# Kernel tuning notes

Hardware: AMD Instinct MI355X
Metric: run time of the kernel (lower is better)

The kernel has to match this reference:

```python
import jax, jax.numpy as jnp
import numpy as np
import math

N = 1000            # proposals
C = 91              # classes incl. background (class 0)
K = 100             # num_detections per class
SCORE_TH = 0.05
NMS_TH = 0.5
MIN_SIZE = 1.0
WX, WY, WW, WH = 10.0, 10.0, 5.0, 5.0   # reg_weights
BBOX_CLIP = math.log(1000.0 / 16.0)


def setup_inputs() -> dict:
    key = jax.random.key(0)
    k1, k2, k3, k4, k5, k6 = jax.random.split(key, 6)
    class_logit = jax.random.normal(k1, (N, C), jnp.float32)
    box_regression = jax.random.normal(k2, (N, C * 4), jnp.float32)
    H, W = 800, 1333
    x1 = jax.random.uniform(k3, (N,)) * (W - 64)
    y1 = jax.random.uniform(k4, (N,)) * (H - 64)
    bw = 16.0 + jax.random.uniform(k5, (N,)) * 240.0
    bh = 16.0 + jax.random.uniform(k6, (N,)) * 240.0
    proposal = jnp.stack([x1, y1, jnp.minimum(x1 + bw, W), jnp.minimum(y1 + bh, H)], axis=1)
    return {"class_logit": class_logit, "box_regression": box_regression,
            "proposal": proposal, "image_h": H, "image_w": W}


def _decode(delta, boxes):
    # delta: [N,4], boxes: [N,4] xyxy -> decoded xyxy (BoxCoder.decode)
    widths = boxes[:, 2] - boxes[:, 0]
    heights = boxes[:, 3] - boxes[:, 1]
    ctr_x = boxes[:, 0] + 0.5 * widths
    ctr_y = boxes[:, 1] + 0.5 * heights
    dx = delta[:, 0] / WX
    dy = delta[:, 1] / WY
    dw = jnp.minimum(delta[:, 2] / WW, BBOX_CLIP)
    dh = jnp.minimum(delta[:, 3] / WH, BBOX_CLIP)
    pcx = dx * widths + ctr_x
    pcy = dy * heights + ctr_y
    pw = jnp.exp(dw) * widths
    ph = jnp.exp(dh) * heights
    return jnp.stack([pcx - 0.5 * pw, pcy - 0.5 * ph,
                      pcx + 0.5 * pw, pcy + 0.5 * ph], axis=1)


def _iou(a, b):
    # a: [N,4], b: [M,4] -> [N,M]
    area_a = (a[:, 2] - a[:, 0]) * (a[:, 3] - a[:, 1])
    area_b = (b[:, 2] - b[:, 0]) * (b[:, 3] - b[:, 1])
    lt = jnp.maximum(a[:, None, :2], b[None, :, :2])
    rb = jnp.minimum(a[:, None, 2:], b[None, :, 2:])
    wh = jnp.clip(rb - lt, 0.0)
    inter = wh[..., 0] * wh[..., 1]
    union = area_a[:, None] + area_b[None, :] - inter
    return inter / jnp.maximum(union, 1e-6)


def _per_class(score, delta, proposal, image_h, image_w):
    # score: [N], delta: [N,4]
    box = _decode(delta, proposal)
    # process_box: clip to image, remove small
    box = jnp.stack([jnp.clip(box[:, 0], 0.0, image_w), jnp.clip(box[:, 1], 0.0, image_h),
                     jnp.clip(box[:, 2], 0.0, image_w), jnp.clip(box[:, 3], 0.0, image_h)], axis=1)
    bw = box[:, 2] - box[:, 0]
    bh = box[:, 3] - box[:, 1]
    valid = (score >= SCORE_TH) & (bw >= MIN_SIZE) & (bh >= MIN_SIZE)
    mscore = jnp.where(valid, score, -1.0)
    order = jnp.argsort(-mscore)
    sbox = box[order]
    sscore = mscore[order]
    svalid = valid[order]
    iou = _iou(sbox, sbox)  # [N,N]
    idx = jnp.arange(N)

    def body(i, keep):
        sup = (iou[i] > NMS_TH) & keep[i] & (idx > i)
        return keep & jnp.logical_not(sup)

    keep = jax.lax.fori_loop(0, N, body, svalid)
    kept_score = jnp.where(keep, sscore, -1.0)
    topv, topi = jax.lax.top_k(kept_score, K)
    out_valid = topv >= 0.0
    out_score = jnp.where(out_valid, topv, 0.0)
    out_box = jnp.where(out_valid[:, None], sbox[topi], 0.0)
    return out_box, out_score, out_valid


def _inference(class_logit, box_regression, proposal, image_h, image_w):
    pred_score = jax.nn.softmax(class_logit, axis=-1)          # [N,C]
    deltas = box_regression.reshape(N, C, 4)
    scores_c = pred_score[:, 1:].T                             # [C-1,N]
    deltas_c = jnp.transpose(deltas[:, 1:], (1, 0, 2))         # [C-1,N,4]
    boxes, scores, valid = jax.vmap(
        lambda s, d: _per_class(s, d, proposal, image_h, image_w))(scores_c, deltas_c)
    labels = jnp.where(valid, jnp.arange(1, C)[:, None], 0).reshape(-1)
    dets = jnp.concatenate([boxes.reshape(-1, 4), scores.reshape(-1, 1)], axis=1)  # [(C-1)*K,5]
    return dets, labels


def reference(class_logit, box_regression, proposal, image_h, image_w):
    return _inference(class_logit, box_regression, proposal,
                      jnp.float32(image_h), jnp.float32(image_w))
```

## Files before the change

kernel.cpp:

```cpp
#include <hip/hip_runtime.h>
#include <math.h>

#define N_PROP 1000
#define NCLS   91
#define NCM1   90
#define KDET   100
#define SCORE_TH 0.05f
#define NMS_TH   0.5f
#define MIN_SIZE 1.0f
#define BBOX_CLIP 4.135166556742356f

#define WS_CNT_OFF     0
#define WS_KEYS_OFF    384
#define WS_IDXS_OFF    360384
#define WS_BOXES_OFF   720384

__global__ __launch_bounds__(128) void zero_kernel(int* __restrict__ counters) {
    int t = threadIdx.x;
    if (t < NCM1) counters[t] = 0;
}

__global__ __launch_bounds__(256) void fused_decode_kernel(
    const float* __restrict__ logit,
    const float* __restrict__ boxreg,
    const float* __restrict__ proposal,
    const int* __restrict__ ih_p,
    const int* __restrict__ iw_p,
    int* __restrict__ counters,
    float* __restrict__ keys,
    int* __restrict__ idxs,
    float4* __restrict__ boxes) {
    const int gid  = blockIdx.x * blockDim.x + threadIdx.x;
    const int row  = gid >> 6;
    const int lane = gid & 63;
    if (row >= N_PROP) return;

    const float* p = logit + row * NCLS;
    float l0 = p[lane];
    float l1 = (lane + 64 < NCLS) ? p[lane + 64] : -INFINITY;
    float m = fmaxf(l0, l1);
    for (int d = 32; d > 0; d >>= 1) m = fmaxf(m, __shfl_xor(m, d));
    float s = expf(l0 - m) + ((lane + 64 < NCLS) ? expf(l1 - m) : 0.0f);
    for (int d = 32; d > 0; d >>= 1) s += __shfl_xor(s, d);
    const float inv = 1.0f / s;

    const float W = (float)(*iw_p);
    const float H = (float)(*ih_p);
    const float4 pr = *(const float4*)(proposal + row * 4);
    const float w  = pr.z - pr.x, h = pr.w - pr.y;
    const float cx = pr.x + 0.5f * w, cy = pr.y + 0.5f * h;

    const float* br = boxreg + (size_t)row * (NCLS * 4);
    for (int c = lane + 1; c < NCLS; c += 64) {
        float lc = p[c];
        float score = expf(lc - m) * inv;

        const float4 d = *(const float4*)(br + c * 4);
        float dx = d.x / 10.0f;
        float dy = d.y / 10.0f;
        float dw = fminf(d.z / 5.0f, BBOX_CLIP);
        float dh = fminf(d.w / 5.0f, BBOX_CLIP);
        float pcx = dx * w + cx, pcy = dy * h + cy;
        float pw  = expf(dw) * w, ph = expf(dh) * h;
        float x1 = pcx - 0.5f * pw, y1 = pcy - 0.5f * ph;
        float x2 = pcx + 0.5f * pw, y2 = pcy + 0.5f * ph;
        x1 = fminf(fmaxf(x1, 0.0f), W);
        x2 = fminf(fmaxf(x2, 0.0f), W);
        y1 = fminf(fmaxf(y1, 0.0f), H);
        y2 = fminf(fmaxf(y2, 0.0f), H);

        bool valid = (score >= SCORE_TH) && ((x2 - x1) >= MIN_SIZE) && ((y2 - y1) >= MIN_SIZE);
        if (valid) {
            int cm1 = c - 1;
            int pos = atomicAdd(&counters[cm1], 1);
            if ((unsigned)pos < N_PROP) {
                int o = cm1 * N_PROP + pos;
                keys[o]  = score;
                idxs[o]  = row;
                boxes[o] = make_float4(x1, y1, x2, y2);
            }
        }
    }
}

__global__ __launch_bounds__(64) void nms_kernel(
    const int* __restrict__ counters,
    const float* __restrict__ keys,
    const int* __restrict__ idxs,
    const float4* __restrict__ boxes,
    float* __restrict__ out) {
    const int cm1 = blockIdx.x;
    const int tid = threadIdx.x;

    __shared__ float  s_key[N_PROP];
    __shared__ int    s_idx[N_PROP];
    __shared__ float4 s_box[N_PROP];
    __shared__ float  s_skey[N_PROP];
    __shared__ float4 s_sbox[N_PROP];
    __shared__ int    s_keep[N_PROP];
    __shared__ int    s_outpos[KDET];
    __shared__ int    s_nout;

    int V = counters[cm1];
    if (V > N_PROP) V = N_PROP;
    if (V < 0) V = 0;

    for (int t = tid; t < V; t += 64) {
        int o = cm1 * N_PROP + t;
        s_key[t] = keys[o];
        s_idx[t] = idxs[o];
        s_box[t] = boxes[o];
    }
    __syncthreads();

    for (int t = tid; t < V; t += 64) {
        float kt = s_key[t];
        int   it = s_idx[t];
        int rank = 0;
        for (int j = 0; j < V; ++j) {
            float kj = s_key[j];
            rank += (kj > kt) || (kj == kt && s_idx[j] < it);
        }
        s_skey[rank] = kt;
        s_sbox[rank] = s_box[t];
        s_keep[rank] = 1;
    }
    __syncthreads();

    for (int i = 0; i + 1 < V; ++i) {
        if (s_keep[i]) {
            float4 bi = s_sbox[i];
            float areai = (bi.z - bi.x) * (bi.w - bi.y);
            for (int t = i + 1 + tid; t < V; t += 64) {
                if (s_keep[t]) {
                    float4 bj = s_sbox[t];
                    float lx = fmaxf(bi.x, bj.x), ly = fmaxf(bi.y, bj.y);
                    float rx = fminf(bi.z, bj.z), ry = fminf(bi.w, bj.w);
                    float iw = fmaxf(rx - lx, 0.0f), ihh = fmaxf(ry - ly, 0.0f);
                    float inter = iw * ihh;
                    float areaj = (bj.z - bj.x) * (bj.w - bj.y);
                    float uni = areai + areaj - inter;
                    float iou = inter / fmaxf(uni, 1e-6f);
                    if (iou > NMS_TH) s_keep[t] = 0;
                }
            }
        }
        __syncthreads();
    }

    if (tid == 0) {
        int cnt = 0;
        for (int t = 0; t < V && cnt < KDET; ++t)
            if (s_keep[t]) s_outpos[cnt++] = t;
        s_nout = cnt;
    }
    __syncthreads();
    const int nout = s_nout;

    float* dets   = out;
    float* labels = out + NCM1 * KDET * 5;
    const int rowbase = cm1 * KDET;
    for (int t = tid; t < KDET; t += 64) {
        float x1 = 0.f, y1 = 0.f, x2 = 0.f, y2 = 0.f, sc = 0.f, lb = 0.f;
        if (t < nout) {
            int p = s_outpos[t];
            float4 b = s_sbox[p];
            x1 = b.x; y1 = b.y; x2 = b.z; y2 = b.w;
            sc = s_skey[p];
            lb = (float)(cm1 + 1);
        }
        float* r = dets + (size_t)(rowbase + t) * 5;
        r[0] = x1; r[1] = y1; r[2] = x2; r[3] = y2; r[4] = sc;
        labels[rowbase + t] = lb;
    }
}

extern "C" void kernel_launch(void* const* d_in, const int* in_sizes, int n_in,
                              void* d_out, int out_size, void* d_ws, size_t ws_size,
                              hipStream_t stream) {
    const float* logit    = (const float*)d_in[0];
    const float* boxreg   = (const float*)d_in[1];
    const float* proposal = (const float*)d_in[2];
    const int*   ih       = (const int*)d_in[3];
    const int*   iw       = (const int*)d_in[4];

    char* ws = (char*)d_ws;
    int*    counters = (int*)(ws + WS_CNT_OFF);
    float*  keys     = (float*)(ws + WS_KEYS_OFF);
    int*    idxs     = (int*)(ws + WS_IDXS_OFF);
    float4* boxes    = (float4*)(ws + WS_BOXES_OFF);

    zero_kernel<<<1, 128, 0, stream>>>(counters);
    fused_decode_kernel<<<250, 256, 0, stream>>>(logit, boxreg, proposal, ih, iw,
                                                 counters, keys, idxs, boxes);
    nms_kernel<<<NCM1, 64, 0, stream>>>(counters, keys, idxs, boxes, (float*)d_out);
}
```

Before: 84.73 us.

## Fuse per-class decode into NMS kernel, precompute softmax stats separately

Splits the softmax into a small stats kernel that stores the per-row max and inverse sum. A per-class kernel then decodes, filters and compacts candidates directly into shared memory with shared atomics before running NMS. This removes the zero kernel, the global atomics and the global workspace round trip for keys, indices and boxes. NMS block size also doubles from 64 to 128 threads. In exchange each class block does strided global reads of logits and box regressions (one element per row), which coalesce poorly.

```diff
diff --git a/kernel.cpp b/kernel.cpp
--- a/kernel.cpp
+++ b/kernel.cpp
@@ -10,31 +10,13 @@
 #define MIN_SIZE 1.0f
 #define BBOX_CLIP 4.135166556742356f
 
-#define WS_CNT_OFF     0
-#define WS_KEYS_OFF    384
-#define WS_IDXS_OFF    360384
-#define WS_BOXES_OFF   720384
 
-__global__ __launch_bounds__(128) void zero_kernel(int* __restrict__ counters) {
-    int t = threadIdx.x;
-    if (t < NCM1) counters[t] = 0;
-}
-
-__global__ __launch_bounds__(256) void fused_decode_kernel(
-    const float* __restrict__ logit,
-    const float* __restrict__ boxreg,
-    const float* __restrict__ proposal,
-    const int* __restrict__ ih_p,
-    const int* __restrict__ iw_p,
-    int* __restrict__ counters,
-    float* __restrict__ keys,
-    int* __restrict__ idxs,
-    float4* __restrict__ boxes) {
+__global__ __launch_bounds__(256) void stats_kernel(const float* __restrict__ logit,
+                                                    float* __restrict__ stats) {
     const int gid  = blockIdx.x * blockDim.x + threadIdx.x;
     const int row  = gid >> 6;
     const int lane = gid & 63;
     if (row >= N_PROP) return;
-
     const float* p = logit + row * NCLS;
     float l0 = p[lane];
     float l1 = (lane + 64 < NCLS) ? p[lane + 64] : -INFINITY;
@@ -42,20 +24,48 @@
     for (int d = 32; d > 0; d >>= 1) m = fmaxf(m, __shfl_xor(m, d));
     float s = expf(l0 - m) + ((lane + 64 < NCLS) ? expf(l1 - m) : 0.0f);
     for (int d = 32; d > 0; d >>= 1) s += __shfl_xor(s, d);
-    const float inv = 1.0f / s;
+    if (lane == 0) {
+        stats[row] = m;
+        stats[N_PROP + row] = 1.0f / s;
+    }
+}
+
+__global__ __launch_bounds__(128) void class_kernel(
+    const float* __restrict__ logit,
+    const float* __restrict__ boxreg,
+    const float* __restrict__ proposal,
+    const int* __restrict__ ih_p,
+    const int* __restrict__ iw_p,
+    const float* __restrict__ stats,
+    float* __restrict__ out) {
+    const int cm1 = blockIdx.x;
+    const int c   = cm1 + 1;
+    const int tid = threadIdx.x;
+
+    __shared__ float  s_key[N_PROP];
+    __shared__ int    s_idx[N_PROP];
+    __shared__ float4 s_box[N_PROP];
+    __shared__ float  s_skey[N_PROP];
+    __shared__ float4 s_sbox[N_PROP];
+    __shared__ int    s_keep[N_PROP];
+    __shared__ int    s_outpos[KDET];
+    __shared__ int    s_cnt, s_nout;
+
+    if (tid == 0) s_cnt = 0;
+    __syncthreads();
 
     const float W = (float)(*iw_p);
     const float H = (float)(*ih_p);
-    const float4 pr = *(const float4*)(proposal + row * 4);
-    const float w  = pr.z - pr.x, h = pr.w - pr.y;
-    const float cx = pr.x + 0.5f * w, cy = pr.y + 0.5f * h;
 
-    const float* br = boxreg + (size_t)row * (NCLS * 4);
-    for (int c = lane + 1; c < NCLS; c += 64) {
-        float lc = p[c];
-        float score = expf(lc - m) * inv;
+    for (int i = tid; i < N_PROP; i += 128) {
+        float lc    = logit[i * NCLS + c];
+        float score = expf(lc - stats[i]) * stats[N_PROP + i];
 
-        const float4 d = *(const float4*)(br + c * 4);
+        const float4 pr = *(const float4*)(proposal + i * 4);
+        float w  = pr.z - pr.x, h = pr.w - pr.y;
+        float cx = pr.x + 0.5f * w, cy = pr.y + 0.5f * h;
+
+        const float4 d = *(const float4*)(boxreg + (size_t)i * (NCLS * 4) + c * 4);
         float dx = d.x / 10.0f;
         float dy = d.y / 10.0f;
         float dw = fminf(d.z / 5.0f, BBOX_CLIP);
@@ -71,49 +81,16 @@
 
         bool valid = (score >= SCORE_TH) && ((x2 - x1) >= MIN_SIZE) && ((y2 - y1) >= MIN_SIZE);
         if (valid) {
-            int cm1 = c - 1;
-            int pos = atomicAdd(&counters[cm1], 1);
-            if ((unsigned)pos < N_PROP) {
-                int o = cm1 * N_PROP + pos;
-                keys[o]  = score;
-                idxs[o]  = row;
-                boxes[o] = make_float4(x1, y1, x2, y2);
-            }
+            int pos = atomicAdd(&s_cnt, 1);
+            s_key[pos] = score;
+            s_idx[pos] = i;
+            s_box[pos] = make_float4(x1, y1, x2, y2);
         }
     }
-}
+    __syncthreads();
+    const int V = s_cnt;
 
-__global__ __launch_bounds__(64) void nms_kernel(
-    const int* __restrict__ counters,
-    const float* __restrict__ keys,
-    const int* __restrict__ idxs,
-    const float4* __restrict__ boxes,
-    float* __restrict__ out) {
-    const int cm1 = blockIdx.x;
-    const int tid = threadIdx.x;
-
-    __shared__ float  s_key[N_PROP];
-    __shared__ int    s_idx[N_PROP];
-    __shared__ float4 s_box[N_PROP];
-    __shared__ float  s_skey[N_PROP];
-    __shared__ float4 s_sbox[N_PROP];
-    __shared__ int    s_keep[N_PROP];
-    __shared__ int    s_outpos[KDET];
-    __shared__ int    s_nout;
-
-    int V = counters[cm1];
-    if (V > N_PROP) V = N_PROP;
-    if (V < 0) V = 0;
-
-    for (int t = tid; t < V; t += 64) {
-        int o = cm1 * N_PROP + t;
-        s_key[t] = keys[o];
-        s_idx[t] = idxs[o];
-        s_box[t] = boxes[o];
-    }
-    __syncthreads();
-
-    for (int t = tid; t < V; t += 64) {
+    for (int t = tid; t < V; t += 128) {
         float kt = s_key[t];
         int   it = s_idx[t];
         int rank = 0;
@@ -131,7 +108,7 @@
         if (s_keep[i]) {
             float4 bi = s_sbox[i];
             float areai = (bi.z - bi.x) * (bi.w - bi.y);
-            for (int t = i + 1 + tid; t < V; t += 64) {
+            for (int t = i + 1 + tid; t < V; t += 128) {
                 if (s_keep[t]) {
                     float4 bj = s_sbox[t];
                     float lx = fmaxf(bi.x, bj.x), ly = fmaxf(bi.y, bj.y);
@@ -160,14 +137,14 @@
     float* dets   = out;
     float* labels = out + NCM1 * KDET * 5;
     const int rowbase = cm1 * KDET;
-    for (int t = tid; t < KDET; t += 64) {
+    for (int t = tid; t < KDET; t += 128) {
         float x1 = 0.f, y1 = 0.f, x2 = 0.f, y2 = 0.f, sc = 0.f, lb = 0.f;
         if (t < nout) {
             int p = s_outpos[t];
             float4 b = s_sbox[p];
             x1 = b.x; y1 = b.y; x2 = b.z; y2 = b.w;
             sc = s_skey[p];
-            lb = (float)(cm1 + 1);
+            lb = (float)c;
         }
         float* r = dets + (size_t)(rowbase + t) * 5;
         r[0] = x1; r[1] = y1; r[2] = x2; r[3] = y2; r[4] = sc;
@@ -183,15 +160,9 @@
     const float* proposal = (const float*)d_in[2];
     const int*   ih       = (const int*)d_in[3];
     const int*   iw       = (const int*)d_in[4];
+    float* stats = (float*)d_ws;
 
-    char* ws = (char*)d_ws;
-    int*    counters = (int*)(ws + WS_CNT_OFF);
-    float*  keys     = (float*)(ws + WS_KEYS_OFF);
-    int*    idxs     = (int*)(ws + WS_IDXS_OFF);
-    float4* boxes    = (float4*)(ws + WS_BOXES_OFF);
-
-    zero_kernel<<<1, 128, 0, stream>>>(counters);
-    fused_decode_kernel<<<250, 256, 0, stream>>>(logit, boxreg, proposal, ih, iw,
-                                                 counters, keys, idxs, boxes);
-    nms_kernel<<<NCM1, 64, 0, stream>>>(counters, keys, idxs, boxes, (float*)d_out);
+    stats_kernel<<<250, 256, 0, stream>>>(logit, stats);
+    class_kernel<<<NCM1, 128, 0, stream>>>(logit, boxreg, proposal, ih, iw,
+                                           stats, (float*)d_out);
 }
```

Result: no change. 85.16 us (+0.5%).
